# Optimization experiments

Hardware: AMD Instinct MI355X
Metric: run time of the kernel (lower is better)

## Reference

```python
import jax, jax.numpy as jnp
import numpy as np

B, C, H, W = 16, 256, 128, 512
MINW, MINH, AF, HS = 128, 32, 256, 256


def _conv1d(x, w, b, pad):
    # x (B, Cin, L), w (Cout, Cin, K) -> (B, Cout, L)
    y = jax.lax.conv_general_dilated(x, w, (1,), [(pad, pad)],
                                     dimension_numbers=('NCH', 'OIH', 'NCH'))
    return y + b[None, :, None]


def setup_inputs() -> dict:
    key = jax.random.key(0)
    ks = jax.random.split(key, 22)
    def p(i, shape, s=0.05):
        return jax.random.normal(ks[i], shape, jnp.float32) * s
    return dict(
        features=jax.random.normal(ks[0], (B, C, H, W), jnp.float32),
        prev_attn_weights=jax.random.uniform(ks[1], (B, H), jnp.float32),
        coverage_vector=jax.random.uniform(ks[2], (B, H), jnp.float32) * 2.0,
        hidden=jax.random.normal(ks[3], (2, 1, B, HS), jnp.float32),
        dw_w=p(4, (MINW, 1)), dw_b=p(5, (1,)),
        enc_w=p(6, (C, AF)), enc_b=p(7, (AF,)),
        conv_w=p(8, (16, 2, 15)), conv_b=p(9, (16,)),
        dcb_w=p(10, (16, AF)), dcb_b=p(11, (AF,)),
        hid_w=p(12, (HS, AF)), hid_b=p(13, (AF,)),
        align_w=p(14, (AF, 1)), align_b=p(15, (1,)),
        convd_w=p(16, (AF, AF, 5)), convd_b=p(17, (AF,)),
        dh_w=p(18, (MINH, 1)), dh_b=p(19, (1,)),
        dec_w=p(20, (HS + AF, 2)), dec_b=p(21, (2,)),
    )


def reference(features, prev_attn_weights, coverage_vector, hidden,
              dw_w, dw_b, enc_w, enc_b, conv_w, conv_b, dcb_w, dcb_b,
              hid_w, hid_b, align_w, align_b, convd_w, convd_b,
              dh_w, dh_b, dec_w, dec_b):
    b, c, h, w = features.shape
    # AdaptiveMaxPool2d((None, MINW)): W divisible by MINW -> uniform windows
    pooled = features.reshape(b, c, h, MINW, w // MINW).max(-1)   # (B,C,H,MINW)
    h_feat = (pooled @ dw_w + dw_b)[..., 0]                       # (B,C,H)
    s = jnp.einsum('bch,cf->bhf', h_feat, enc_w) + enc_b          # (B,H,AF)
    # location + clamped coverage, InstanceNorm1d (no affine, eps=1e-5)
    cat = jnp.stack([prev_attn_weights,
                     jnp.clip(coverage_vector, 0.0, 1.0)], axis=1)  # (B,2,H)
    mu = cat.mean(-1, keepdims=True)
    var = cat.var(-1, keepdims=True)
    cat = (cat - mu) * jax.lax.rsqrt(var + 1e-5)
    cb = _conv1d(cat, conv_w, conv_b, 7)                          # (B,16,H)
    s = s + jnp.einsum('bkh,kf->bhf', cb, dcb_w) + dcb_b
    hh = hidden[0]                                                # (1,B,HS) = LSTM h
    s = s + (jnp.einsum('lbh,hf->lbf', hh, hid_w) + hid_b).transpose(1, 0, 2)  # (B,1,AF) bcast
    s = jnp.tanh(s)
    align = s @ align_w + align_b                                 # (B,H,1)
    attn = jax.nn.softmax(align, axis=1)[..., 0]                  # (B,H)
    context = jnp.einsum('bchw,bh->bcw', features, attn)          # (B,C,W)
    # learned stop decision
    d = jax.nn.relu(_conv1d(s.transpose(0, 2, 1), convd_w, convd_b, 2))  # (B,AF,H)
    d = d.reshape(b, AF, MINH, h // MINH).max(-1)                 # AdaptiveMaxPool1d(MINH)
    d = jax.nn.relu(d @ dh_w + dh_b)[..., 0]                      # (B,AF)
    d = jnp.concatenate([hh[0], d], axis=1)                       # (B,HS+AF)
    decision = d @ dec_w + dec_b                                  # (B,2)
    return context, attn, decision
```

## Files before the change

kernel.cpp:

```cpp
#include <hip/hip_runtime.h>
#include <hip/hip_bf16.h>
#include <math.h>

#define B_ 16
#define C_ 256
#define H_ 128
#define W_ 512
#define AF_ 256
#define HS_ 256

typedef float f4v __attribute__((ext_vector_type(4)));

__global__ void k_pre_pool(const float* __restrict__ feat,
                           const float* __restrict__ dw_w,
                           const float* __restrict__ dw_b,
                           const float* __restrict__ convd_w,
                           const float* __restrict__ hidden,
                           const float* __restrict__ hid_w,
                           const float* __restrict__ hid_b,
                           float* __restrict__ hf, float* __restrict__ w2,
                           float* __restrict__ hv) {
  int bid = blockIdx.x, tid = threadIdx.x;
  if (bid < 256) {
    int f = bid;
#pragma unroll
    for (int q = 0; q < 5; ++q) {
      int r = q * 256 + tid;
      w2[(size_t)r * 256 + f] = convd_w[(size_t)f * 1280 + r];
    }
  } else if (bid < 272) {
    int b = bid - 256;
    const float* hh = hidden + b * HS_;
    float acc = hid_b[tid];
    for (int k = 0; k < HS_; ++k) acc = fmaf(hh[k], hid_w[k * AF_ + tid], acc);
    hv[b * AF_ + tid] = acc;
  } else {
    int wid = (bid - 272) * 4 + (tid >> 6);
    int lane = tid & 63;
    const f4v* row = reinterpret_cast<const f4v*>(feat) + (size_t)wid * 128;
    f4v a = __builtin_nontemporal_load(row + lane);
    f4v b = __builtin_nontemporal_load(row + lane + 64);
    float m0 = fmaxf(fmaxf(a.x, a.y), fmaxf(a.z, a.w));
    float m1 = fmaxf(fmaxf(b.x, b.y), fmaxf(b.z, b.w));
    float p = m0 * dw_w[lane] + m1 * dw_w[lane + 64];
#pragma unroll
    for (int off = 32; off > 0; off >>= 1) p += __shfl_down(p, off, 64);
    if (lane == 0) hf[wid] = p + dw_b[0];
  }
}

__global__ void k_sbuild(const float* __restrict__ pa,
                         const float* __restrict__ cv,
                         const float* __restrict__ hf,
                         const float* __restrict__ enc_w, const float* __restrict__ enc_b,
                         const float* __restrict__ conv_w, const float* __restrict__ conv_b,
                         const float* __restrict__ dcb_w, const float* __restrict__ dcb_b,
                         const float* __restrict__ hv,
                         const float* __restrict__ align_w, const float* __restrict__ align_b,
                         float* __restrict__ sbuf, float* __restrict__ alignv) {
  __shared__ float cat[2][H_];
  __shared__ float stats[4];
  __shared__ float cbl[4][16];
  __shared__ float red[4][4];
  int bidx = blockIdx.x;
  int b = bidx >> 5;
  int h0 = (bidx & 31) * 4;
  int tid = threadIdx.x;

  if (tid < H_) {
    cat[0][tid] = pa[b * H_ + tid];
    float x = cv[b * H_ + tid];
    cat[1][tid] = fminf(fmaxf(x, 0.f), 1.f);
  }
  __syncthreads();
  if (tid < 2) {
    float s = 0.f, s2 = 0.f;
    for (int t = 0; t < H_; ++t) { float x = cat[tid][t]; s += x; s2 += x * x; }
    float mu = s / (float)H_;
    float var = s2 / (float)H_ - mu * mu;
    stats[tid * 2] = mu;
    stats[tid * 2 + 1] = rsqrtf(var + 1e-5f);
  }
  __syncthreads();
  {
    int ch = tid >> 7, t = tid & 127;
    cat[ch][t] = (cat[ch][t] - stats[ch * 2]) * stats[ch * 2 + 1];
  }
  __syncthreads();
  if (tid < 64) {
    int k = tid & 15, j = tid >> 4;
    int h = h0 + j;
    float acc = conv_b[k];
    for (int c2 = 0; c2 < 2; ++c2)
      for (int t = 0; t < 15; ++t) {
        int hh = h + t - 7;
        if (hh >= 0 && hh < H_) acc += cat[c2][hh] * conv_w[(k * 2 + c2) * 15 + t];
      }
    cbl[j][k] = acc;
  }
  __syncthreads();

  int f = tid;
  float base = enc_b[f] + dcb_b[f] + hv[b * AF_ + f];
  float acc[4];
#pragma unroll
  for (int j = 0; j < 4; ++j) {
    float a = base;
#pragma unroll
    for (int k = 0; k < 16; ++k) a = fmaf(cbl[j][k], dcb_w[k * AF_ + f], a);
    acc[j] = a;
  }
  const float* hfb = hf + (size_t)(b * C_) * H_ + h0;
  for (int c = 0; c < C_; ++c) {
    float w = enc_w[c * AF_ + f];
#pragma unroll
    for (int j = 0; j < 4; ++j) acc[j] = fmaf(hfb[c * H_ + j], w, acc[j]);
  }
  float aw = align_w[f];
  int wvi = tid >> 6, lane = tid & 63;
#pragma unroll
  for (int j = 0; j < 4; ++j) {
    float s = tanhf(acc[j]);
    sbuf[(size_t)(b * H_ + h0 + j) * AF_ + f] = s;
    float v = s * aw;
#pragma unroll
    for (int off = 32; off > 0; off >>= 1) v += __shfl_down(v, off, 64);
    if (lane == 0) red[wvi][j] = v;
  }
  __syncthreads();
  if (tid < 4)
    alignv[b * H_ + h0 + tid] =
        red[0][tid] + red[1][tid] + red[2][tid] + red[3][tid] + align_b[0];
}

__global__ void k_softmax(const float* __restrict__ alignv, float* __restrict__ attn) {
  __shared__ float redm[2], reds[2];
  int b = blockIdx.x, t = threadIdx.x;
  float v = alignv[b * H_ + t];
  float m = v;
#pragma unroll
  for (int off = 32; off > 0; off >>= 1) m = fmaxf(m, __shfl_down(m, off, 64));
  if ((t & 63) == 0) redm[t >> 6] = m;
  __syncthreads();
  float mm = fmaxf(redm[0], redm[1]);
  float e = expf(v - mm);
  float s = e;
#pragma unroll
  for (int off = 32; off > 0; off >>= 1) s += __shfl_down(s, off, 64);
  if ((t & 63) == 0) reds[t >> 6] = s;
  __syncthreads();
  attn[b * H_ + t] = e / (reds[0] + reds[1]);
}

__global__ void k_ctx_dconv(const float* __restrict__ feat, const float* __restrict__ attn,
                            const float* __restrict__ sbuf, const float* __restrict__ w2,
                            const float* __restrict__ convd_b,
                            float* __restrict__ dpool, float* __restrict__ ctx) {
  __shared__ float sw[12][AF_];
  int bidx = blockIdx.x;
  int tid = threadIdx.x;
  if (bidx < 256) {
    int b = bidx >> 4;
    int h0 = (bidx & 15) * 8;
    int f = tid;
    for (int rr = 0; rr < 12; ++rr) {
      int h = h0 - 2 + rr;
      sw[rr][f] = (h >= 0 && h < H_) ? sbuf[(size_t)(b * H_ + h) * AF_ + f] : 0.f;
    }
    __syncthreads();
    float acc[8];
#pragma unroll
    for (int j = 0; j < 8; ++j) acc[j] = 0.f;
    for (int c = 0; c < C_; ++c) {
      float sr[12];
#pragma unroll
      for (int rr = 0; rr < 12; ++rr) sr[rr] = sw[rr][c];
      const float* wp = w2 + (size_t)c * 5 * 256 + f;
#pragma unroll
      for (int t = 0; t < 5; ++t) {
        float wvv = wp[t * 256];
#pragma unroll
        for (int j = 0; j < 8; ++j) acc[j] = fmaf(sr[j + t], wvv, acc[j]);
      }
    }
    float bias = convd_b[f];
#pragma unroll
    for (int j = 0; j < 8; ++j) acc[j] = fmaxf(acc[j] + bias, 0.f);
    float p0 = fmaxf(fmaxf(acc[0], acc[1]), fmaxf(acc[2], acc[3]));
    float p1 = fmaxf(fmaxf(acc[4], acc[5]), fmaxf(acc[6], acc[7]));
    int m0 = h0 >> 2;
    dpool[(size_t)(b * 32 + m0) * AF_ + f] = p0;
    dpool[(size_t)(b * 32 + m0 + 1) * AF_ + f] = p1;
  } else {
    int cb = 2303 - bidx;
    int b = cb >> 7;
    int c0 = (cb & 127) * 2;
    float* at = &sw[0][0];
    if (tid < H_) at[tid] = attn[b * H_ + tid];
    __syncthreads();
    int c = c0 + (tid >> 7);
    int wq = tid & 127;
    const f4v* f4 = reinterpret_cast<const f4v*>(feat) +
                    (size_t)(b * C_ + c) * H_ * (W_ / 4) + wq;
    f4v acc = (f4v){0.f, 0.f, 0.f, 0.f};
#pragma unroll 4
    for (int h = 0; h < H_; ++h) {
      f4v x = __builtin_nontemporal_load(f4 + (size_t)h * (W_ / 4));
      float a = at[h];
      acc.x += x.x * a; acc.y += x.y * a; acc.z += x.z * a; acc.w += x.w * a;
    }
    __builtin_nontemporal_store(acc,
        reinterpret_cast<f4v*>(ctx) + (size_t)(b * C_ + c) * (W_ / 4) + wq);
  }
}

__global__ void k_decision(const float* __restrict__ dpool, const float* __restrict__ hidden,
                           const float* __restrict__ dh_w, const float* __restrict__ dh_b,
                           const float* __restrict__ dec_w, const float* __restrict__ dec_b,
                           float* __restrict__ dec_out) {
  __shared__ float ddl[AF_];
  __shared__ float red[4];
  int b = blockIdx.x, tid = threadIdx.x;
  float acc = dh_b[0];
  for (int m = 0; m < 32; ++m) acc = fmaf(dpool[(size_t)(b * 32 + m) * AF_ + tid], dh_w[m], acc);
  ddl[tid] = fmaxf(acc, 0.f);
  __syncthreads();
  int col = tid >> 7, kk = tid & 127;
  float a = 0.f;
#pragma unroll
  for (int q = 0; q < 4; ++q) {
    int idx = kk + 128 * q;
    float x = (idx < 256) ? hidden[b * HS_ + idx] : ddl[idx - 256];
    a = fmaf(x, dec_w[idx * 2 + col], a);
  }
#pragma unroll
  for (int off = 32; off > 0; off >>= 1) a += __shfl_down(a, off, 64);
  if ((tid & 63) == 0) red[tid >> 6] = a;
  __syncthreads();
  if (tid < 2) dec_out[b * 2 + tid] = red[tid * 2] + red[tid * 2 + 1] + dec_b[tid];
}

extern "C" void kernel_launch(void* const* d_in, const int* in_sizes, int n_in,
                              void* d_out, int out_size, void* d_ws, size_t ws_size,
                              hipStream_t stream) {
  const float* feat    = (const float*)d_in[0];
  const float* pa      = (const float*)d_in[1];
  const float* cv      = (const float*)d_in[2];
  const float* hidden  = (const float*)d_in[3];
  const float* dw_w    = (const float*)d_in[4];
  const float* dw_b    = (const float*)d_in[5];
  const float* enc_w   = (const float*)d_in[6];
  const float* enc_b   = (const float*)d_in[7];
  const float* conv_w  = (const float*)d_in[8];
  const float* conv_b  = (const float*)d_in[9];
  const float* dcb_w   = (const float*)d_in[10];
  const float* dcb_b   = (const float*)d_in[11];
  const float* hid_w   = (const float*)d_in[12];
  const float* hid_b   = (const float*)d_in[13];
  const float* align_w = (const float*)d_in[14];
  const float* align_b = (const float*)d_in[15];
  const float* convd_w = (const float*)d_in[16];
  const float* convd_b = (const float*)d_in[17];
  const float* dh_w    = (const float*)d_in[18];
  const float* dh_b    = (const float*)d_in[19];
  const float* dec_w   = (const float*)d_in[20];
  const float* dec_b   = (const float*)d_in[21];

  float* out  = (float*)d_out;
  float* ctx  = out;
  float* attn = out + 2097152;
  float* dec  = out + 2097152 + 2048;

  float* ws     = (float*)d_ws;
  float* hf     = ws;
  float* sbuf   = ws + 524288;
  float* hv     = ws + 1048576;
  float* alignv = ws + 1052672;
  float* w2     = ws + 1054720;
  float* dpool  = ws + 1382400;

  k_pre_pool<<<131344, 256, 0, stream>>>(feat, dw_w, dw_b, convd_w, hidden,
                                         hid_w, hid_b, hf, w2, hv);
  k_sbuild<<<512, 256, 0, stream>>>(pa, cv, hf, enc_w, enc_b, conv_w, conv_b,
                                    dcb_w, dcb_b, hv, align_w, align_b, sbuf, alignv);
  k_softmax<<<16, 128, 0, stream>>>(alignv, attn);
  k_ctx_dconv<<<2304, 256, 0, stream>>>(feat, attn, sbuf, w2, convd_b, dpool, ctx);
  k_decision<<<16, 256, 0, stream>>>(dpool, hidden, dh_w, dh_b, dec_w, dec_b, dec);
}
```

Baseline: 396.7 us.

## Fuse softmax into context kernel and halve rows per sbuild block

Removes the standalone softmax launch. Each context block now recomputes the softmax over its batch's 128 alignment scores, and only the c0==0 blocks write attn. k_sbuild handles 2 rows per block instead of 4, doubling the grid to 1024 blocks for more parallelism, and the context loop unroll goes from 4 to 8. The cost is redundant softmax work in every context block and more total enc_w reads in sbuild.

```diff
diff --git a/kernel.cpp b/kernel.cpp
--- a/kernel.cpp
+++ b/kernel.cpp
@@ -60,11 +60,11 @@
                          float* __restrict__ sbuf, float* __restrict__ alignv) {
   __shared__ float cat[2][H_];
   __shared__ float stats[4];
-  __shared__ float cbl[4][16];
-  __shared__ float red[4][4];
+  __shared__ float cbl[2][16];
+  __shared__ float red[4][2];
   int bidx = blockIdx.x;
-  int b = bidx >> 5;
-  int h0 = (bidx & 31) * 4;
+  int b = bidx >> 6;
+  int h0 = (bidx & 63) * 2;
   int tid = threadIdx.x;
 
   if (tid < H_) {
@@ -87,7 +87,7 @@
     cat[ch][t] = (cat[ch][t] - stats[ch * 2]) * stats[ch * 2 + 1];
   }
   __syncthreads();
-  if (tid < 64) {
+  if (tid < 32) {
     int k = tid & 15, j = tid >> 4;
     int h = h0 + j;
     float acc = conv_b[k];
@@ -102,9 +102,9 @@
 
   int f = tid;
   float base = enc_b[f] + dcb_b[f] + hv[b * AF_ + f];
-  float acc[4];
-#pragma unroll
-  for (int j = 0; j < 4; ++j) {
+  float acc[2];
+#pragma unroll
+  for (int j = 0; j < 2; ++j) {
     float a = base;
 #pragma unroll
     for (int k = 0; k < 16; ++k) a = fmaf(cbl[j][k], dcb_w[k * AF_ + f], a);
@@ -114,12 +114,12 @@
   for (int c = 0; c < C_; ++c) {
     float w = enc_w[c * AF_ + f];
 #pragma unroll
-    for (int j = 0; j < 4; ++j) acc[j] = fmaf(hfb[c * H_ + j], w, acc[j]);
+    for (int j = 0; j < 2; ++j) acc[j] = fmaf(hfb[c * H_ + j], w, acc[j]);
   }
   float aw = align_w[f];
   int wvi = tid >> 6, lane = tid & 63;
 #pragma unroll
-  for (int j = 0; j < 4; ++j) {
+  for (int j = 0; j < 2; ++j) {
     float s = tanhf(acc[j]);
     sbuf[(size_t)(b * H_ + h0 + j) * AF_ + f] = s;
     float v = s * aw;
@@ -128,34 +128,17 @@
     if (lane == 0) red[wvi][j] = v;
   }
   __syncthreads();
-  if (tid < 4)
+  if (tid < 2)
     alignv[b * H_ + h0 + tid] =
         red[0][tid] + red[1][tid] + red[2][tid] + red[3][tid] + align_b[0];
 }
 
-__global__ void k_softmax(const float* __restrict__ alignv, float* __restrict__ attn) {
-  __shared__ float redm[2], reds[2];
-  int b = blockIdx.x, t = threadIdx.x;
-  float v = alignv[b * H_ + t];
-  float m = v;
-#pragma unroll
-  for (int off = 32; off > 0; off >>= 1) m = fmaxf(m, __shfl_down(m, off, 64));
-  if ((t & 63) == 0) redm[t >> 6] = m;
-  __syncthreads();
-  float mm = fmaxf(redm[0], redm[1]);
-  float e = expf(v - mm);
-  float s = e;
-#pragma unroll
-  for (int off = 32; off > 0; off >>= 1) s += __shfl_down(s, off, 64);
-  if ((t & 63) == 0) reds[t >> 6] = s;
-  __syncthreads();
-  attn[b * H_ + t] = e / (reds[0] + reds[1]);
-}
-
-__global__ void k_ctx_dconv(const float* __restrict__ feat, const float* __restrict__ attn,
+__global__ void k_ctx_dconv(const float* __restrict__ feat,
+                            const float* __restrict__ alignv,
                             const float* __restrict__ sbuf, const float* __restrict__ w2,
                             const float* __restrict__ convd_b,
-                            float* __restrict__ dpool, float* __restrict__ ctx) {
+                            float* __restrict__ dpool, float* __restrict__ attn,
+                            float* __restrict__ ctx) {
   __shared__ float sw[12][AF_];
   int bidx = blockIdx.x;
   int tid = threadIdx.x;
@@ -196,14 +179,35 @@
     int b = cb >> 7;
     int c0 = (cb & 127) * 2;
     float* at = &sw[0][0];
-    if (tid < H_) at[tid] = attn[b * H_ + tid];
+    float* r1 = &sw[1][0];
+    float* r2 = &sw[1][8];
+    int wv = tid >> 6, lane = tid & 63;
+    float v = (tid < H_) ? alignv[b * H_ + tid] : -1e30f;
+    float m = v;
+#pragma unroll
+    for (int off = 32; off > 0; off >>= 1) m = fmaxf(m, __shfl_down(m, off, 64));
+    if (lane == 0) r1[wv] = m;
+    __syncthreads();
+    float mm = fmaxf(fmaxf(r1[0], r1[1]), fmaxf(r1[2], r1[3]));
+    float e = expf(v - mm);
+    float s = e;
+#pragma unroll
+    for (int off = 32; off > 0; off >>= 1) s += __shfl_down(s, off, 64);
+    if (lane == 0) r2[wv] = s;
+    __syncthreads();
+    float S = r2[0] + r2[1] + r2[2] + r2[3];
+    if (tid < H_) {
+      float a = e / S;
+      at[tid] = a;
+      if (c0 == 0) attn[b * H_ + tid] = a;
+    }
     __syncthreads();
     int c = c0 + (tid >> 7);
     int wq = tid & 127;
     const f4v* f4 = reinterpret_cast<const f4v*>(feat) +
                     (size_t)(b * C_ + c) * H_ * (W_ / 4) + wq;
     f4v acc = (f4v){0.f, 0.f, 0.f, 0.f};
-#pragma unroll 4
+#pragma unroll 8
     for (int h = 0; h < H_; ++h) {
       f4v x = __builtin_nontemporal_load(f4 + (size_t)h * (W_ / 4));
       float a = at[h];
@@ -281,9 +285,9 @@
 
   k_pre_pool<<<131344, 256, 0, stream>>>(feat, dw_w, dw_b, convd_w, hidden,
                                          hid_w, hid_b, hf, w2, hv);
-  k_sbuild<<<512, 256, 0, stream>>>(pa, cv, hf, enc_w, enc_b, conv_w, conv_b,
-                                    dcb_w, dcb_b, hv, align_w, align_b, sbuf, alignv);
-  k_softmax<<<16, 128, 0, stream>>>(alignv, attn);
-  k_ctx_dconv<<<2304, 256, 0, stream>>>(feat, attn, sbuf, w2, convd_b, dpool, ctx);
+  k_sbuild<<<1024, 256, 0, stream>>>(pa, cv, hf, enc_w, enc_b, conv_w, conv_b,
+                                     dcb_w, dcb_b, hv, align_w, align_b, sbuf, alignv);
+  k_ctx_dconv<<<2304, 256, 0, stream>>>(feat, alignv, sbuf, w2, convd_b,
+                                        dpool, attn, ctx);
   k_decision<<<16, 256, 0, stream>>>(dpool, hidden, dh_w, dh_b, dec_w, dec_b, dec);
 }
```

Measured after the change: 402.1 us. No clear change (+1.4%).
